# Kernel optimization log

Measured on AMD Instinct MI355X. Metric: run time of the kernel, lower is better.

Reference implementation:

```python
import jax, jax.numpy as jnp
import numpy as np

B, CI, GEN, CON, CO, FAC = 32768, 128, 512, 256, 64, 128
CLIP = 5.0
# h_0 layout: [gen_state, con_state, co_mean, co_std, gen_input, factor]
SPLITS = [GEN, GEN + CON, GEN + CON + CO, GEN + CON + 2 * CO, GEN + CON + 3 * CO]


def _gru(x, h, Wih, bih, Whh, bhh, H):
    # x_all = x @ Wih.T + bih ; chunks z, r, n
    xa = x @ Wih.T + bih
    xz, xr, xn = jnp.split(xa, 3, axis=1)
    ha = h @ Whh[: 2 * H].T + bhh[: 2 * H]
    hz, hr = jnp.split(ha, 2, axis=1)
    z = jax.nn.sigmoid(xz + hz)
    r = jax.nn.sigmoid(xr + hr)
    # note: torch code computes (r * hidden) @ W_n.T (left-assoc * and @)
    hn = (r * h) @ Whh[2 * H :].T + bhh[2 * H :]
    n = jnp.tanh(xn + hn)
    h_new = z * h + (1.0 - z) * n
    return jnp.clip(h_new, -CLIP, CLIP)


def setup_inputs() -> dict:
    key = jax.random.key(0)
    ks = jax.random.split(key, 12)
    rn = lambda k, shape, scale: (jax.random.normal(k, shape, jnp.float32) * scale)
    return {
        "input": rn(ks[0], (B, 2 * CI), 1.0),
        "h_0": rn(ks[1], (B, GEN + CON + 3 * CO + FAC), 1.0),
        "eps": rn(ks[2], (B, CO), 1.0),
        "gen_Wih": rn(ks[3], (3 * GEN, CO), 1.0 / np.sqrt(CO)),
        "gen_bih": jnp.concatenate([jnp.ones(2 * GEN, jnp.float32), jnp.zeros(GEN, jnp.float32)]),
        "gen_Whh": rn(ks[4], (3 * GEN, GEN), 1.0 / np.sqrt(GEN)),
        "gen_bhh": jnp.zeros(3 * GEN, jnp.float32),
        "con_Wih": rn(ks[5], (3 * CON, 2 * CI + FAC), 1.0 / np.sqrt(2 * CI + FAC)),
        "con_bih": jnp.concatenate([jnp.ones(2 * CON, jnp.float32), jnp.zeros(CON, jnp.float32)]),
        "con_Whh": rn(ks[6], (3 * CON, CON), 1.0 / np.sqrt(CON)),
        "con_bhh": jnp.zeros(3 * CON, jnp.float32),
        "fac_W": rn(ks[7], (FAC, GEN), 1.0 / np.sqrt(GEN)),
        "co_W": rn(ks[8], (2 * CO, CON), 1.0 / np.sqrt(CON)),
        "co_b": jnp.zeros(2 * CO, jnp.float32),
    }


def reference(input, h_0, eps, gen_Wih, gen_bih, gen_Whh, gen_bhh,
              con_Wih, con_bih, con_Whh, con_bhh, fac_W, co_W, co_b):
    gen_state, con_state, co_mean, co_std, gen_input, factor = jnp.split(h_0, SPLITS, axis=1)
    # controller path (use_con=True): dropout is identity (rate=0 / eval)
    con_input = jnp.concatenate([input, factor], axis=1)
    con_state = _gru(con_input, con_state, con_Wih, con_bih, con_Whh, con_bhh, CON)
    co_params = con_state @ co_W.T + co_b
    co_mean, co_logvar = jnp.split(co_params, 2, axis=1)
    co_std = jnp.exp(0.5 * co_logvar)  # sqrt(exp(logvar))
    gen_input = co_mean + co_std * eps  # rsample (sample_posteriors=True)
    gen_state = _gru(gen_input, gen_state, gen_Wih, gen_bih, gen_Whh, gen_bhh, GEN)
    # kernel-normalized linear: L2-normalize each output row over in_features
    norm = jnp.sqrt(jnp.sum(fac_W * fac_W, axis=1, keepdims=True))
    normed_W = fac_W / jnp.maximum(norm, 1e-12)
    factor = gen_state @ normed_W.T
    return jnp.concatenate([gen_state, con_state, co_mean, co_std, gen_input, factor], axis=1)
```

## Files before the change

kernel.cpp:

```cpp
#include <hip/hip_runtime.h>


typedef short  s16x8 __attribute__((ext_vector_type(8)));
typedef float  f32x4 __attribute__((ext_vector_type(4)));
typedef unsigned short ush;

#define OUTP 1088
#define NROW 32768

__device__ __forceinline__ int swz(int k, int row) {
  return (k & ~63) | ((k & 63) ^ ((row & 7) << 3));
}
__device__ __forceinline__ ush f2bf(float f) {
  union { float f; unsigned int u; } v; v.f = f;
  unsigned int u = v.u;
  return (ush)((u + 0x7FFFu + ((u >> 16) & 1u)) >> 16);
}
__device__ __forceinline__ float bf2f(ush b) {
  union { unsigned int u; float f; } v; v.u = ((unsigned int)b) << 16;
  return v.f;
}
__device__ __forceinline__ float sigm(float x) { return 1.f / (1.f + __expf(-x)); }
__device__ __forceinline__ float tanh_(float x) { return 2.f / (1.f + __expf(-2.f * x)) - 1.f; }

__device__ __forceinline__ f32x4 mfma16(s16x8 a, s16x8 b, f32x4 c) {
  return __builtin_amdgcn_mfma_f32_16x16x32_bf16(a, b, c, 0, 0, 0);
}
__device__ __forceinline__ s16x8 ldb8(const ush* p) {
  return *reinterpret_cast<const s16x8*>(p);
}
__device__ __forceinline__ void gld16(const ush* g, ush* l) {
  __builtin_amdgcn_global_load_lds(
      (const __attribute__((address_space(1))) unsigned int*)g,
      (__attribute__((address_space(3))) unsigned int*)l, 16, 0, 0);
}
__device__ __forceinline__ ushort4 pack4(float4 a) {
  ushort4 o; o.x = f2bf(a.x); o.y = f2bf(a.y); o.z = f2bf(a.z); o.w = f2bf(a.w);
  return o;
}

__global__ void prepA_kernel(const float* __restrict__ in, const float* __restrict__ h0,
                             ush* __restrict__ Acon, ush* __restrict__ Agen) {
  int t = blockIdx.x * 256 + threadIdx.x;
  int row = t / 144, c = t % 144;
  if (c < 80) {
    int c8 = c * 8;
    const float* src;
    if (c8 < 256)      src = &in[(size_t)row * 256 + c8];
    else if (c8 < 384) src = &h0[(size_t)row * OUTP + 960 + (c8 - 256)];
    else               src = &h0[(size_t)row * OUTP + 512 + (c8 - 384)];
    float4 a = *reinterpret_cast<const float4*>(src);
    float4 b = *reinterpret_cast<const float4*>(src + 4);
    ushort4* d = reinterpret_cast<ushort4*>(&Acon[(size_t)row * 640 + swz(c8, row)]);
    d[0] = pack4(a); d[1] = pack4(b);
  } else {
    int c8 = (c - 80) * 8;
    float4 a = *reinterpret_cast<const float4*>(&h0[(size_t)row * OUTP + c8]);
    float4 b = *reinterpret_cast<const float4*>(&h0[(size_t)row * OUTP + c8 + 4]);
    ushort4* d = reinterpret_cast<ushort4*>(&Agen[(size_t)row * 576 + swz(64 + c8, row)]);
    d[0] = pack4(a); d[1] = pack4(b);
  }
}

__global__ void packBcon_kernel(const float* __restrict__ wih, const float* __restrict__ whh,
                                ush* __restrict__ B1, ush* __restrict__ B2) {
  int r = blockIdx.x;
  int c4 = threadIdx.x * 4;
  float4 v = (c4 < 384) ? *reinterpret_cast<const float4*>(&wih[(size_t)r * 384 + c4])
                        : *reinterpret_cast<const float4*>(&whh[(size_t)r * 256 + (c4 - 384)]);
  int pc = swz(c4, r);
  ush* dst = (r < 512) ? &B1[(size_t)r * 640 + pc] : &B2[(size_t)(r - 512) * 640 + pc];
  *reinterpret_cast<ushort4*>(dst) = pack4(v);
}

__global__ void packBgen_kernel(const float* __restrict__ wih, const float* __restrict__ whh,
                                ush* __restrict__ B1, ush* __restrict__ B2) {
  int r = blockIdx.x;
  int c4 = threadIdx.x * 4;
  float4 v = (c4 < 64) ? *reinterpret_cast<const float4*>(&wih[(size_t)r * 64 + c4])
                       : *reinterpret_cast<const float4*>(&whh[(size_t)r * 512 + (c4 - 64)]);
  int pc = swz(c4, r);
  ush* dst = (r < 1024) ? &B1[(size_t)r * 576 + pc] : &B2[(size_t)(r - 1024) * 576 + pc];
  *reinterpret_cast<ushort4*>(dst) = pack4(v);
}

__global__ void cvtco_kernel(const float* __restrict__ src, ush* __restrict__ dst) {
  int i = blockIdx.x * 256 + threadIdx.x;
  int row = i >> 6, c4 = (i & 63) * 4;
  float4 v = *reinterpret_cast<const float4*>(&src[(size_t)row * 256 + c4]);
  *reinterpret_cast<ushort4*>(&dst[(size_t)row * 256 + swz(c4, row)]) = pack4(v);
}

__global__ void facnorm_kernel(const float* __restrict__ w, ush* __restrict__ dst) {
  int row = blockIdx.x;
  int lane = threadIdx.x;
  float v[8]; float s = 0.f;
  #pragma unroll
  for (int i = 0; i < 8; ++i) { v[i] = w[row * 512 + lane * 8 + i]; s += v[i] * v[i]; }
  #pragma unroll
  for (int off = 32; off; off >>= 1) s += __shfl_xor(s, off);
  float scale = 1.f / fmaxf(sqrtf(s), 1e-12f);
  int pc = swz(lane * 8, row);
  #pragma unroll
  for (int i = 0; i < 8; ++i) dst[row * 512 + pc + i] = f2bf(v[i] * scale);
}

__global__ void rsample_kernel(const float* __restrict__ eps, float* __restrict__ out,
                               ush* __restrict__ Agen) {
  int t = blockIdx.x * 256 + threadIdx.x;
  int m = t >> 6, j = t & 63;
  float mean = out[(size_t)m * OUTP + 768 + j];
  float sd   = out[(size_t)m * OUTP + 832 + j];
  float g = mean + sd * eps[(size_t)m * 64 + j];
  out[(size_t)m * OUTP + 896 + j] = g;
  Agen[(size_t)m * 576 + (j ^ ((m & 7) << 3))] = f2bf(g);
}

template<int EPI, int KTOT, int KA1, int SA1, int SA2, int SB,
         int NT, int NHALF, int SAH, int OOFS, int SHN>
__global__ __launch_bounds__(512, 2) void gemmD_kernel(
    const ush* __restrict__ A1, const ush* __restrict__ A2,
    const ush* __restrict__ B,
    const float* __restrict__ bih, const float* __restrict__ bhh,
    const ush* __restrict__ Ah,
    const ush* __restrict__ zbuf,
    ush* __restrict__ st1, ush* __restrict__ st2,
    float* __restrict__ out)
{
  __shared__ __align__(16) ush S[2 * 2 * 128 * 64];
  const int nwg = gridDim.x;
  const int wg = (blockIdx.x & 7) * (nwg >> 3) + (blockIdx.x >> 3);
  const int mt = wg / NT, nt = wg % NT;
  const int m0 = mt * 128, n0 = nt * 128;
  const int tid = threadIdx.x;
  const int wv = tid >> 6, lane = tid & 63;
  const int ln = lane & 15, lk = lane >> 4;
  const int wm = wv >> 2, wn = wv & 3;
  const int srow = lane >> 3;
  const int scol = (lane & 7) * 8;
  const int xs = (ln & 7) << 3;
  constexpr int NK = KTOT / 64;

  f32x4 acc[4][2] = {};

  const int ar0 = wv * 16 + srow, ar1 = wv * 16 + 8 + srow;
  const ush* a1p0 = A1 + (size_t)(m0 + ar0) * SA1 + scol;
  const ush* a1p1 = A1 + (size_t)(m0 + ar1) * SA1 + scol;
  const ush* a2p0 = A2 + (size_t)(m0 + ar0) * SA2 + scol;
  const ush* a2p1 = A2 + (size_t)(m0 + ar1) * SA2 + scol;
  const ush* bp0  = B  + (size_t)(n0 + ar0) * SB  + scol;
  const ush* bp1  = B  + (size_t)(n0 + ar1) * SB  + scol;
  ush* ldsA0 = &S[(wv * 16) * 64];
  ush* ldsA1 = &S[(wv * 16 + 8) * 64];

  auto STAGE = [&](int t, int b) {
    const int k0 = t * 64;
    ush* As = ldsA0 + b * 16384;
    ush* As1 = ldsA1 + b * 16384;
    if (KA1 >= KTOT || k0 < KA1) {
      gld16(a1p0 + k0, As);
      gld16(a1p1 + k0, As1);
    } else {
      gld16(a2p0 + (k0 - KA1), As);
      gld16(a2p1 + (k0 - KA1), As1);
    }
    gld16(bp0 + k0, As + 8192);
    gld16(bp1 + k0, As1 + 8192);
  };

  STAGE(0, 0);
  #pragma unroll
  for (int t = 0; t < NK; ++t) {
    asm volatile("s_waitcnt vmcnt(0)" ::: "memory");
    __builtin_amdgcn_s_barrier();
    if (t + 1 < NK) STAGE(t + 1, (t + 1) & 1);
    const ush* As = &S[(t & 1) * 16384];
    const ush* Bs = As + 8192;
    __builtin_amdgcn_s_setprio(1);
    #pragma unroll
    for (int kk2 = 0; kk2 < 2; ++kk2) {
      const int kb = (kk2 * 32 + lk * 8) ^ xs;
      s16x8 af[4], bf[2];
      #pragma unroll
      for (int i = 0; i < 4; ++i) af[i] = ldb8(&As[(wm * 64 + i * 16 + ln) * 64 + kb]);
      #pragma unroll
      for (int j = 0; j < 2; ++j) bf[j] = ldb8(&Bs[(wn * 32 + j * 16 + ln) * 64 + kb]);
      #pragma unroll
      for (int i = 0; i < 4; ++i)
        #pragma unroll
        for (int j = 0; j < 2; ++j)
          acc[i][j] = mfma16(af[i], bf[j], acc[i][j]);
    }
    __builtin_amdgcn_s_setprio(0);
  }

  __syncthreads();

  ush* Ls = S;

  if constexpr (EPI == 0) {
    const bool isz = (n0 < NHALF);
    #pragma unroll
    for (int i = 0; i < 4; ++i) {
      #pragma unroll
      for (int j = 0; j < 2; ++j) {
        const int jl = wn * 32 + j * 16 + ln;
        const int jg = n0 + jl;
        const float bb = bih[jg] + bhh[jg];
        #pragma unroll
        for (int r = 0; r < 4; ++r) {
          const int rl = wm * 64 + i * 16 + lk * 4 + r;
          float sv = sigm(acc[i][j][r] + bb);
          if (!isz) sv *= bf2f(Ah[(size_t)(m0 + rl) * SAH + swz(jg - NHALF, rl)]);
          Ls[rl * 128 + (jl ^ ((rl & 7) << 3))] = f2bf(sv);
        }
      }
    }
    __syncthreads();
    #pragma unroll
    for (int q = 0; q < 4; ++q) {
      int idx = q * 512 + tid;
      int r = idx >> 4, c8 = (idx & 15) * 8;
      float4 v = *reinterpret_cast<const float4*>(&Ls[r * 128 + (c8 ^ ((r & 7) << 3))]);
      if (isz) *reinterpret_cast<float4*>(&st1[(size_t)(m0 + r) * NHALF + n0 + c8]) = v;
      else     *reinterpret_cast<float4*>(&st2[(size_t)(m0 + r) * NHALF +
                                               swz(n0 - NHALF + c8, r)]) = v;
    }
  } else {
    #pragma unroll
    for (int i = 0; i < 4; ++i) {
      #pragma unroll
      for (int j = 0; j < 2; ++j) {
        const int jl = wn * 32 + j * 16 + ln;
        const int jg = n0 + jl;
        const float bb = bih[2 * NHALF + jg] + bhh[2 * NHALF + jg];
        #pragma unroll
        for (int r = 0; r < 4; ++r) {
          const int rl = wm * 64 + i * 16 + lk * 4 + r;
          const size_t m = (size_t)(m0 + rl);
          float n = tanh_(acc[i][j][r] + bb);
          float z = bf2f(zbuf[m * NHALF + jg]);
          float h = bf2f(Ah[m * SAH + swz(jg, rl)]);
          float hv = fminf(fmaxf(z * h + (1.f - z) * n, -5.f), 5.f);
          Ls[rl * 128 + (jl ^ ((rl & 7) << 3))] = f2bf(hv);
        }
      }
    }
    __syncthreads();
    #pragma unroll
    for (int q = 0; q < 4; ++q) {
      int idx = q * 512 + tid;
      int r = idx >> 4, c8 = (idx & 15) * 8;
      union { float4 f; ush u[8]; } U;
      U.f = *reinterpret_cast<const float4*>(&Ls[r * 128 + (c8 ^ ((r & 7) << 3))]);
      *reinterpret_cast<float4*>(&st1[(size_t)(m0 + r) * SHN + swz(n0 + c8, r)]) = U.f;
      float4 o0 = { bf2f(U.u[0]), bf2f(U.u[1]), bf2f(U.u[2]), bf2f(U.u[3]) };
      float4 o1 = { bf2f(U.u[4]), bf2f(U.u[5]), bf2f(U.u[6]), bf2f(U.u[7]) };
      float* ob = &out[(size_t)(m0 + r) * OUTP + OOFS + n0 + c8];
      *reinterpret_cast<float4*>(ob) = o0;
      *reinterpret_cast<float4*>(ob + 4) = o1;
    }
  }
}

template<int EPI, int KTOT, int KA1, int SA1, int SA2, int SB,
         int NT, int NHALF, int SAH, int OOFS, int SHN>
__global__ __launch_bounds__(256, 4) void gemm_kernel(
    const ush* __restrict__ A1, const ush* __restrict__ A2,
    const ush* __restrict__ B,
    const float* __restrict__ bih, const float* __restrict__ bhh,
    const ush* __restrict__ Ah,
    const ush* __restrict__ zbuf,
    ush* __restrict__ st1, ush* __restrict__ st2,
    float* __restrict__ out)
{
  __shared__ ush S[2 * 128 * 64];
  const int nwg = gridDim.x;
  const int wg = (blockIdx.x & 7) * (nwg >> 3) + (blockIdx.x >> 3);
  const int mt = wg / NT, nt = wg % NT;
  const int m0 = mt * 128, n0 = nt * 128;
  const int tid = threadIdx.x;
  const int w = tid >> 6, lane = tid & 63;
  const int ln = lane & 15, lk = lane >> 4;
  const int wm = w >> 1, wn = w & 1;
  const int srow = lane >> 3;
  const int scol = (lane & 7) * 8;
  constexpr int NK = KTOT / 64;
  const int xs = (ln & 7) << 3;

  f32x4 acc[4][4] = {};
  ush* As = S;
  ush* Bs = S + 8192;

  #pragma unroll
  for (int ks = 0; ks < NK; ++ks) {
    const int k0 = ks * 64;
    const ush* Ab; size_t sa; int kk;
    if (KA1 >= KTOT || k0 < KA1) { Ab = A1; sa = SA1; kk = k0; }
    else                         { Ab = A2; sa = SA2; kk = k0 - KA1; }
    #pragma unroll
    for (int p = 0; p < 4; ++p) {
      int r0 = p * 32 + w * 8;
      gld16(Ab + (size_t)(m0 + r0 + srow) * sa + kk + scol, &As[r0 * 64]);
    }
    #pragma unroll
    for (int p = 0; p < 4; ++p) {
      int r0 = p * 32 + w * 8;
      gld16(B + (size_t)(n0 + r0 + srow) * SB + k0 + scol, &Bs[r0 * 64]);
    }
    asm volatile("s_waitcnt vmcnt(0)" ::: "memory");
    __syncthreads();
    #pragma unroll
    for (int kk2 = 0; kk2 < 2; ++kk2) {
      const int kb = (kk2 * 32 + lk * 8) ^ xs;
      s16x8 af[4], bf[4];
      #pragma unroll
      for (int i = 0; i < 4; ++i) af[i] = ldb8(&As[(wm * 64 + i * 16 + ln) * 64 + kb]);
      #pragma unroll
      for (int i = 0; i < 4; ++i) bf[i] = ldb8(&Bs[(wn * 64 + i * 16 + ln) * 64 + kb]);
      #pragma unroll
      for (int i = 0; i < 4; ++i)
        #pragma unroll
        for (int j = 0; j < 4; ++j)
          acc[i][j] = mfma16(af[i], bf[j], acc[i][j]);
    }
    __syncthreads();
  }

  if constexpr (EPI == 2) {
    #pragma unroll
    for (int i = 0; i < 4; ++i) {
      #pragma unroll
      for (int j = 0; j < 4; ++j) {
        const int jg = n0 + wn * 64 + j * 16 + ln;
        const float bb = bih[jg];
        #pragma unroll
        for (int r = 0; r < 4; ++r) {
          const size_t m = (size_t)(m0 + wm * 64 + i * 16 + lk * 4 + r);
          float v = acc[i][j][r] + bb;
          if (jg < 64) out[m * OUTP + 768 + jg] = v;
          else         out[m * OUTP + 832 + (jg - 64)] = __expf(0.5f * v);
        }
      }
    }
  } else {
    #pragma unroll
    for (int i = 0; i < 4; ++i)
      #pragma unroll
      for (int j = 0; j < 4; ++j) {
        const int jg = n0 + wn * 64 + j * 16 + ln;
        #pragma unroll
        for (int r = 0; r < 4; ++r)
          out[(size_t)(m0 + wm * 64 + i * 16 + lk * 4 + r) * OUTP + 960 + jg] =
              acc[i][j][r];
      }
  }
}

extern "C" void kernel_launch(void* const* d_in, const int* in_sizes, int n_in,
                              void* d_out, int out_size, void* d_ws, size_t ws_size,
                              hipStream_t stream) {
  const float* input   = (const float*)d_in[0];
  const float* h0      = (const float*)d_in[1];
  const float* eps     = (const float*)d_in[2];
  const float* gen_Wih = (const float*)d_in[3];
  const float* gen_bih = (const float*)d_in[4];
  const float* gen_Whh = (const float*)d_in[5];
  const float* gen_bhh = (const float*)d_in[6];
  const float* con_Wih = (const float*)d_in[7];
  const float* con_bih = (const float*)d_in[8];
  const float* con_Whh = (const float*)d_in[9];
  const float* con_bhh = (const float*)d_in[10];
  const float* fac_W   = (const float*)d_in[11];
  const float* co_W    = (const float*)d_in[12];
  const float* co_b    = (const float*)d_in[13];
  float* out = (float*)d_out;

  ush* ws = (ush*)d_ws;
  ush* A_gen  = ws;
  ush* A_con  = A_gen + (size_t)NROW * 576;
  ush* z_con  = A_con + (size_t)NROW * 640;
  ush* rh_con = z_con + (size_t)NROW * 256;
  ush* B1c    = rh_con + (size_t)NROW * 256;
  ush* B2c    = B1c + 512 * 640;
  ush* B1g    = B2c + 256 * 640;
  ush* B2g    = B1g + 1024 * 576;
  ush* coWb   = B2g + 512 * 576;
  ush* facWn  = coWb + 128 * 256;
  ush* z_gen  = A_con;
  ush* rh_gen = z_con;

  packBcon_kernel<<<768, 160, 0, stream>>>(con_Wih, con_Whh, B1c, B2c);
  packBgen_kernel<<<1536, 144, 0, stream>>>(gen_Wih, gen_Whh, B1g, B2g);
  cvtco_kernel<<<32, 256, 0, stream>>>(co_W, coWb);
  facnorm_kernel<<<128, 64, 0, stream>>>(fac_W, facWn);
  prepA_kernel<<<18432, 256, 0, stream>>>(input, h0, A_con, A_gen);

  gemmD_kernel<0, 640, 640, 640, 640, 640, 4, 256, 640, 0, 0>
      <<<1024, 512, 0, stream>>>(A_con, A_con, B1c, con_bih, con_bhh,
                                 A_con + 384, nullptr, z_con, rh_con, out);
  gemmD_kernel<1, 640, 384, 640, 256, 640, 2, 256, 640, 512, 640>
      <<<512, 512, 0, stream>>>(A_con, rh_con, B2c, con_bih, con_bhh,
                                A_con + 384, z_con, A_con + 384, nullptr, out);
  gemm_kernel<2, 256, 256, 640, 640, 256, 1, 64, 640, 0, 0>
      <<<256, 256, 0, stream>>>(A_con + 384, A_con + 384, coWb, co_b, co_b,
                                nullptr, nullptr, nullptr, nullptr, out);
  rsample_kernel<<<8192, 256, 0, stream>>>(eps, out, A_gen);

  gemmD_kernel<0, 576, 576, 576, 576, 576, 8, 512, 576, 0, 0>
      <<<2048, 512, 0, stream>>>(A_gen, A_gen, B1g, gen_bih, gen_bhh,
                                 A_gen + 64, nullptr, z_gen, rh_gen, out);
  gemmD_kernel<1, 576, 64, 576, 512, 576, 4, 512, 576, 0, 576>
      <<<1024, 512, 0, stream>>>(A_gen, rh_gen, B2g, gen_bih, gen_bhh,
                                 A_gen + 64, z_gen, A_gen + 64, nullptr, out);
  gemm_kernel<3, 512, 512, 576, 576, 512, 1, 0, 576, 960, 0>
      <<<256, 256, 0, stream>>>(A_gen + 64, A_gen + 64, facWn, gen_bih, gen_bhh,
                                nullptr, nullptr, nullptr, nullptr, out);
}
```

Measured before the change: 293.3 us.

## Replace double-buffered GEMM main loop with single-buffered LDS for higher occupancy

The four GRU GEMM launches now use a single LDS buffer instead of two. Each K step loads its tile, waits, syncs, computes, then syncs again. This halves shared memory per block. The launch bound is also raised from 2 to 8 so more workgroups can be resident, hoping that occupancy hides global latency instead of the explicit prefetch. In exchange, load and compute no longer overlap within a block, each step gets an extra barrier, and the tighter register cap may cause spills.

```diff
diff --git a/kernel.cpp b/kernel.cpp
--- a/kernel.cpp
+++ b/kernel.cpp
@@ -118,7 +118,7 @@
 
 template<int EPI, int KTOT, int KA1, int SA1, int SA2, int SB,
          int NT, int NHALF, int SAH, int OOFS, int SHN>
-__global__ __launch_bounds__(512, 2) void gemmD_kernel(
+__global__ __launch_bounds__(512, 8) void gemmS_kernel(
     const ush* __restrict__ A1, const ush* __restrict__ A2,
     const ush* __restrict__ B,
     const float* __restrict__ bih, const float* __restrict__ bhh,
@@ -127,7 +127,7 @@
     ush* __restrict__ st1, ush* __restrict__ st2,
     float* __restrict__ out)
 {
-  __shared__ __align__(16) ush S[2 * 2 * 128 * 64];
+  __shared__ __align__(16) ush S[2 * 128 * 64];
   const int nwg = gridDim.x;
   const int wg = (blockIdx.x & 7) * (nwg >> 3) + (blockIdx.x >> 3);
   const int mt = wg / NT, nt = wg % NT;
@@ -153,29 +153,22 @@
   ush* ldsA0 = &S[(wv * 16) * 64];
   ush* ldsA1 = &S[(wv * 16 + 8) * 64];
 
-  auto STAGE = [&](int t, int b) {
-    const int k0 = t * 64;
-    ush* As = ldsA0 + b * 16384;
-    ush* As1 = ldsA1 + b * 16384;
-    if (KA1 >= KTOT || k0 < KA1) {
-      gld16(a1p0 + k0, As);
-      gld16(a1p1 + k0, As1);
-    } else {
-      gld16(a2p0 + (k0 - KA1), As);
-      gld16(a2p1 + (k0 - KA1), As1);
-    }
-    gld16(bp0 + k0, As + 8192);
-    gld16(bp1 + k0, As1 + 8192);
-  };
-
-  STAGE(0, 0);
   #pragma unroll
   for (int t = 0; t < NK; ++t) {
+    const int k0 = t * 64;
+    if (KA1 >= KTOT || k0 < KA1) {
+      gld16(a1p0 + k0, ldsA0);
+      gld16(a1p1 + k0, ldsA1);
+    } else {
+      gld16(a2p0 + (k0 - KA1), ldsA0);
+      gld16(a2p1 + (k0 - KA1), ldsA1);
+    }
+    gld16(bp0 + k0, ldsA0 + 8192);
+    gld16(bp1 + k0, ldsA1 + 8192);
     asm volatile("s_waitcnt vmcnt(0)" ::: "memory");
-    __builtin_amdgcn_s_barrier();
-    if (t + 1 < NK) STAGE(t + 1, (t + 1) & 1);
-    const ush* As = &S[(t & 1) * 16384];
-    const ush* Bs = As + 8192;
+    __syncthreads();
+    const ush* As = S;
+    const ush* Bs = S + 8192;
     __builtin_amdgcn_s_setprio(1);
     #pragma unroll
     for (int kk2 = 0; kk2 < 2; ++kk2) {
@@ -192,9 +185,8 @@
           acc[i][j] = mfma16(af[i], bf[j], acc[i][j]);
     }
     __builtin_amdgcn_s_setprio(0);
+    __syncthreads();
   }
-
-  __syncthreads();
 
   ush* Ls = S;
 
@@ -396,10 +388,10 @@
   facnorm_kernel<<<128, 64, 0, stream>>>(fac_W, facWn);
   prepA_kernel<<<18432, 256, 0, stream>>>(input, h0, A_con, A_gen);
 
-  gemmD_kernel<0, 640, 640, 640, 640, 640, 4, 256, 640, 0, 0>
+  gemmS_kernel<0, 640, 640, 640, 640, 640, 4, 256, 640, 0, 0>
       <<<1024, 512, 0, stream>>>(A_con, A_con, B1c, con_bih, con_bhh,
                                  A_con + 384, nullptr, z_con, rh_con, out);
-  gemmD_kernel<1, 640, 384, 640, 256, 640, 2, 256, 640, 512, 640>
+  gemmS_kernel<1, 640, 384, 640, 256, 640, 2, 256, 640, 512, 640>
       <<<512, 512, 0, stream>>>(A_con, rh_con, B2c, con_bih, con_bhh,
                                 A_con + 384, z_con, A_con + 384, nullptr, out);
   gemm_kernel<2, 256, 256, 640, 640, 256, 1, 64, 640, 0, 0>
@@ -407,10 +399,10 @@
                                 nullptr, nullptr, nullptr, nullptr, out);
   rsample_kernel<<<8192, 256, 0, stream>>>(eps, out, A_gen);
 
-  gemmD_kernel<0, 576, 576, 576, 576, 576, 8, 512, 576, 0, 0>
+  gemmS_kernel<0, 576, 576, 576, 576, 576, 8, 512, 576, 0, 0>
       <<<2048, 512, 0, stream>>>(A_gen, A_gen, B1g, gen_bih, gen_bhh,
                                  A_gen + 64, nullptr, z_gen, rh_gen, out);
-  gemmD_kernel<1, 576, 64, 576, 512, 576, 4, 512, 576, 0, 576>
+  gemmS_kernel<1, 576, 64, 576, 512, 576, 4, 512, 576, 0, 576>
       <<<1024, 512, 0, stream>>>(A_gen, rh_gen, B2g, gen_bih, gen_bhh,
                                  A_gen + 64, z_gen, A_gen + 64, nullptr, out);
   gemm_kernel<3, 512, 512, 576, 576, 512, 1, 0, 576, 960, 0>
```

Result: slower. 364.9 us (+24.4%).
